# Kernel tuning notes

Hardware: AMD Instinct MI355X
Metric: run time of the kernel (lower is better)

Reference implementation:

```python
import jax, jax.numpy as jnp
from jax import lax
import numpy as np

T, B, DIN, NQ = 256, 2048, 128, 16  # hidden_dim == n_qubits (required by module math)


def setup_inputs() -> dict:
    key = jax.random.key(0)
    k1, k2, k3 = jax.random.split(key, 3)
    inputs = jax.random.normal(k1, (T, B, DIN), dtype=jnp.float32)
    # stacked params for the 4 gates: forget, input, update, output
    W = jax.random.normal(k2, (4, NQ, DIN + NQ), dtype=jnp.float32) * 0.1
    b = jnp.zeros((4, NQ), dtype=jnp.float32)
    theta = jax.random.normal(k3, (4, NQ), dtype=jnp.float32)
    return {"inputs": inputs, "W": W, "b": b, "theta": theta}


def reference(inputs, W, b, theta):
    # Analytic simulation of each QGate circuit:
    #   RX(x_i) then RX(theta_i) on wire i  ->  product state, <Z_i> = cos(x_i + theta_i)
    #   CNOT chain (0->1, 1->2, ...): Heisenberg picture maps Z_k -> Z_0 Z_1 ... Z_k,
    Tn, Bn, _ = inputs.shape
    nq = theta.shape[-1]
    h0 = jnp.zeros((Bn, nq), dtype=inputs.dtype)
    c0 = jnp.zeros((Bn, nq), dtype=inputs.dtype)

    def step(carry, x):
        hx, cx = carry
        combined = jnp.concatenate([x, hx], axis=1)              # [B, Din+H]
        z = jnp.einsum('bd,gnd->bgn', combined, W) + b           # [B, 4, nq]
        q = jnp.cumprod(jnp.cos(z + theta), axis=-1)             # quantum gate expectations
        f = jax.nn.sigmoid(q[:, 0])
        i = jax.nn.sigmoid(q[:, 1])
        g = jnp.tanh(q[:, 2])
        o = jax.nn.sigmoid(q[:, 3])
        cx = f * cx + i * g
        hx = o * jnp.tanh(cx)
        return (hx, cx), hx

    (hx, cx), outputs = lax.scan(step, (h0, c0), inputs)
    return outputs, hx, cx
```

## Files before the change

kernel.cpp:

```cpp
#include <hip/hip_runtime.h>
#include <hip/hip_bf16.h>
#include <stdint.h>


#define T_STEPS 256
#define BATCH   2048
#define DIN     128
#define NQ      16
#define DTOT    144
#define NTILE   32
#define ZROW    66

typedef __attribute__((ext_vector_type(8))) short bf16x8;
typedef __attribute__((ext_vector_type(4))) float f32x4;

__device__ __forceinline__ float bf2f(unsigned short u) {
    union { unsigned int i; float f; } v; v.i = ((unsigned int)u) << 16; return v.f;
}
__device__ __forceinline__ unsigned short f2bf(float f) {
    union { float f; unsigned int i; } v; v.f = f;
    unsigned int i = v.i;
    unsigned int r = i + 0x7fffu + ((i >> 16) & 1u);
    return (unsigned short)(r >> 16);
}
__device__ __forceinline__ float ldval(const float* p) { return *p; }
__device__ __forceinline__ float ldval(const unsigned short* p) { return bf2f(*p); }

__device__ __forceinline__ int detect_bf16(const unsigned int* __restrict__ xw, int lane) {
    int cnt = 0;
#pragma unroll
    for (int i = 0; i < 4; ++i) {
        unsigned int w = xw[lane + i * 64];
        unsigned int e = (w >> 7) & 0xFFu;
        cnt += (e >= 100u && e <= 140u) ? 1 : 0;
    }
#pragma unroll
    for (int d = 32; d > 0; d >>= 1) cnt += __shfl_down(cnt, d, 64);
    int tot = __shfl(cnt, 0, 64);
    return (tot >= 140) ? 1 : 0;
}

template <int CTRL>
__device__ __forceinline__ float dpp_sh(float v) {
    int r = __builtin_amdgcn_update_dpp(__builtin_bit_cast(int, 1.0f),
                                        __builtin_bit_cast(int, v),
                                        CTRL, 0xF, 0xF, false);
    return __builtin_bit_cast(float, r);
}
template <int CTRL>
__device__ __forceinline__ float rot16(float v) {
    int r = __builtin_amdgcn_update_dpp(0, __builtin_bit_cast(int, v),
                                        CTRL, 0xF, 0xF, false);
    return __builtin_bit_cast(float, r);
}

__device__ __forceinline__ float dot1(float h, float cur, const float (&Wp)[16]) {
    float h1  = rot16<0x121>(h), h2  = rot16<0x122>(h), h3  = rot16<0x123>(h);
    float h4  = rot16<0x124>(h), h5  = rot16<0x125>(h), h6  = rot16<0x126>(h), h7  = rot16<0x127>(h);
    float h8  = rot16<0x128>(h), h9  = rot16<0x129>(h), h10 = rot16<0x12A>(h), h11 = rot16<0x12B>(h);
    float h12 = rot16<0x12C>(h), h13 = rot16<0x12D>(h), h14 = rot16<0x12E>(h), h15 = rot16<0x12F>(h);
    float a0 = fmaf(Wp[3], h3, fmaf(Wp[2], h2, fmaf(Wp[1], h1, fmaf(Wp[0], h, cur))));
    float a1 = fmaf(Wp[7], h7, fmaf(Wp[6], h6, fmaf(Wp[5], h5, Wp[4] * h4)));
    float a2 = fmaf(Wp[11], h11, fmaf(Wp[10], h10, fmaf(Wp[9], h9, Wp[8] * h8)));
    float a3 = fmaf(Wp[15], h15, fmaf(Wp[14], h14, fmaf(Wp[13], h13, Wp[12] * h12)));
    return (a0 + a1) + (a2 + a3);
}

template <int BASE>
__device__ __forceinline__ float cosprefix(float z) {
    float cz = __cosf(z);
    cz *= dpp_sh<BASE + 1>(cz);
    cz *= dpp_sh<BASE + 2>(cz);
    cz *= dpp_sh<BASE + 4>(cz);
    cz *= dpp_sh<BASE + 8>(cz);
    return cz;
}

__device__ __forceinline__ void tail1(int t, int g, int n, float cz,
                                      float& h, float& c, float& hs, int b,
                                      float kexp, float ksc, float koff,
                                      int a_f, int a_i, int a_g, int a_o,
                                      float* __restrict__ out)
{
    float e = __builtin_amdgcn_exp2f(cz * kexp);
    float rr = __builtin_amdgcn_rcpf(1.f + e);
    float s = fmaf(ksc, rr, koff);

    int si = __builtin_bit_cast(int, s);
    float fv = __builtin_bit_cast(float, __builtin_amdgcn_ds_bpermute(a_f, si));
    float iv = __builtin_bit_cast(float, __builtin_amdgcn_ds_bpermute(a_i, si));
    float gv = __builtin_bit_cast(float, __builtin_amdgcn_ds_bpermute(a_g, si));
    float ov = __builtin_bit_cast(float, __builtin_amdgcn_ds_bpermute(a_o, si));

    c = fmaf(fv, c, iv * gv);
    float e2 = __builtin_amdgcn_exp2f(c * -2.885390082f);
    float tc = fmaf(2.f, __builtin_amdgcn_rcpf(1.f + e2), -1.f);
    h = ov * tc;

    if ((t & 3) == g) hs = h;
    if ((t & 3) == 3)
        out[(size_t)(t - 3 + g) * (BATCH * NQ) + (size_t)b * NQ + n] = hs;
}

template <int BASE, typename InT>
__device__ __forceinline__ void fused_main(
    const InT* __restrict__ x, const InT* __restrict__ W,
    const InT* __restrict__ bv, const InT* __restrict__ th,
    float* __restrict__ out, int bA, int w, int lane,
    const float (&Wp)[16], float (*zt)[ZROW],
    bf16x8 (*wfh)[64], bf16x8 (*wfl)[64])
{
    const int m = lane & 15, quad = lane >> 4;
    const int g = quad, n = m;
    const int bB = bA + 1;
    const float kexp = (g == 2) ? -2.885390082f : -1.442695041f;
    const float ksc  = (g == 2) ? 2.f : 1.f;
    const float koff = (g == 2) ? -1.f : 0.f;
    const int a_f = n << 2, a_i = (16 + n) << 2, a_g = (32 + n) << 2, a_o = (48 + n) << 2;

    if constexpr (sizeof(InT) == 2) {
#pragma unroll
        for (int nb = 0; nb < 4; ++nb)
            wfh[w * 4 + nb][lane] = *(const bf16x8*)((const unsigned short*)W +
                                    (size_t)(nb * 16 + m) * DTOT + w * 32 + quad * 8);
    } else {
#pragma unroll
        for (int nb = 0; nb < 4; ++nb) {
            const float* p = (const float*)W + (size_t)(nb * 16 + m) * DTOT + w * 32 + quad * 8;
            bf16x8 ah, al;
#pragma unroll
            for (int j = 0; j < 8; ++j) {
                float wv = p[j];
                unsigned short hh = f2bf(wv);
                ah[j] = (short)hh;
                al[j] = (short)f2bf(wv - bf2f(hh));
            }
            wfh[w * 4 + nb][lane] = ah;
            wfl[w * 4 + nb][lane] = al;
        }
    }
    const float bias = ldval(bv + lane) + ldval(th + lane);
    __syncthreads();

    const InT* xbase = x + ((size_t)(m & 7) * BATCH + (size_t)(bA + (m >> 3))) * DIN + quad * 8;

    f32x4 rx[8]; bf16x8 rbx[4];
    auto LOAD = [&](int tl) {
        const InT* p = xbase + (size_t)tl * ((size_t)8 * BATCH * DIN);
#pragma unroll
        for (int kt = 0; kt < 4; ++kt) {
            if constexpr (sizeof(InT) == 2) {
                rbx[kt] = *(const bf16x8*)(p + kt * 32);
            } else {
                rx[2 * kt]     = *(const f32x4*)((const float*)p + kt * 32);
                rx[2 * kt + 1] = *(const f32x4*)((const float*)p + kt * 32 + 4);
            }
        }
    };
    auto PRODUCE = [&]() {
        f32x4 acc[4] = {};
#pragma unroll
        for (int kt = 0; kt < 4; ++kt) {
            if constexpr (sizeof(InT) == 2) {
#pragma unroll
                for (int nb = 0; nb < 4; ++nb)
                    acc[nb] = __builtin_amdgcn_mfma_f32_16x16x32_bf16(rbx[kt], wfh[kt * 4 + nb][lane], acc[nb], 0, 0, 0);
            } else {
                bf16x8 ah, al;
#pragma unroll
                for (int j = 0; j < 8; ++j) {
                    float xv = rx[2 * kt + (j >> 2)][j & 3];
                    unsigned short hh = f2bf(xv);
                    ah[j] = (short)hh;
                    al[j] = (short)f2bf(xv - bf2f(hh));
                }
#pragma unroll
                for (int nb = 0; nb < 4; ++nb)
                    acc[nb] = __builtin_amdgcn_mfma_f32_16x16x32_bf16(ah, wfh[kt * 4 + nb][lane], acc[nb], 0, 0, 0);
#pragma unroll
                for (int nb = 0; nb < 4; ++nb)
                    acc[nb] = __builtin_amdgcn_mfma_f32_16x16x32_bf16(al, wfh[kt * 4 + nb][lane], acc[nb], 0, 0, 0);
#pragma unroll
                for (int nb = 0; nb < 4; ++nb)
                    acc[nb] = __builtin_amdgcn_mfma_f32_16x16x32_bf16(ah, wfl[kt * 4 + nb][lane], acc[nb], 0, 0, 0);
            }
        }
#pragma unroll
        for (int nb = 0; nb < 4; ++nb)
#pragma unroll
            for (int r = 0; r < 4; ++r)
                zt[quad * 4 + r][nb * 16 + m] = acc[nb][r];
    };

    float hA = 0.f, cA = 0.f, hsA = 0.f;
    float hB = 0.f, cB = 0.f, hsB = 0.f;
    float zrA[8], zrB[8];

    LOAD(0);
    PRODUCE();
    LOAD(1);
#pragma unroll
    for (int j = 0; j < 8; ++j) zrA[j] = zt[j][lane] + bias;
#pragma unroll
    for (int j = 0; j < 8; ++j) zrB[j] = zt[8 + j][lane] + bias;

    float zA = dot1(hA, zrA[0], Wp);
    float czB = 0.f;

#pragma unroll 1
    for (int tl = 0; tl < NTILE; ++tl) {
        if (tl < NTILE - 1) PRODUCE();
        if (tl < NTILE - 2) LOAD(tl + 2);
#pragma unroll
        for (int j = 0; j < 8; ++j) {
            const int t = tl * 8 + j;
            float czA = cosprefix<BASE>(zA);
            if (j != 0 || tl != 0)
                tail1(t - 1, g, n, czB, hB, cB, hsB, bB,
                      kexp, ksc, koff, a_f, a_i, a_g, a_o, out);
            float zB = dot1(hB, zrB[j], Wp);
            czB = cosprefix<BASE>(zB);
            tail1(t, g, n, czA, hA, cA, hsA, bA,
                  kexp, ksc, koff, a_f, a_i, a_g, a_o, out);
            if (j < 7) zA = dot1(hA, zrA[j + 1], Wp);
        }
        if (tl < NTILE - 1) {
#pragma unroll
            for (int j = 0; j < 8; ++j) zrA[j] = zt[j][lane] + bias;
#pragma unroll
            for (int j = 0; j < 8; ++j) zrB[j] = zt[8 + j][lane] + bias;
            zA = dot1(hA, zrA[0], Wp);
        }
    }
    tail1(T_STEPS - 1, g, n, czB, hB, cB, hsB, bB,
          kexp, ksc, koff, a_f, a_i, a_g, a_o, out);

    if (g == 0) {
        out[(size_t)T_STEPS * BATCH * NQ + (size_t)bA * NQ + n] = hA;
        out[(size_t)T_STEPS * BATCH * NQ + (size_t)BATCH * NQ + (size_t)bA * NQ + n] = cA;
        out[(size_t)T_STEPS * BATCH * NQ + (size_t)bB * NQ + n] = hB;
        out[(size_t)T_STEPS * BATCH * NQ + (size_t)BATCH * NQ + (size_t)bB * NQ + n] = cB;
    }
}

__global__ __launch_bounds__(256, 1) void qlstm_fused(
    const void* __restrict__ x_, const void* __restrict__ W_,
    const void* __restrict__ b_, const void* __restrict__ th_,
    float* __restrict__ out)
{
    __shared__ float  zw[4][16][ZROW];
    __shared__ bf16x8 wfh[16][64];
    __shared__ bf16x8 wfl[16][64];

    const int lane = threadIdx.x & 63;
    const int w    = threadIdx.x >> 6;
    const int bA   = (blockIdx.x * 4 + w) * 2;
    const int n    = lane & 15;

    const int isbf = __builtin_amdgcn_readfirstlane(detect_bf16((const unsigned int*)x_, lane));

    int pr  = __builtin_amdgcn_update_dpp(0, lane, 0x121, 0xF, 0xF, false);
    int p0r = __shfl(pr, 0, 64);
    const int d = (p0r == 1) ? 1 : 15;

    float Wp[16];
    if (isbf) {
        const unsigned short* W = (const unsigned short*)W_;
#pragma unroll
        for (int k = 0; k < 16; ++k)
            Wp[k] = bf2f(W[(size_t)lane * DTOT + DIN + ((n + k * d) & 15)]);
    } else {
        const float* W = (const float*)W_;
#pragma unroll
        for (int k = 0; k < 16; ++k)
            Wp[k] = W[(size_t)lane * DTOT + DIN + ((n + k * d) & 15)];
    }

    int probe = __builtin_amdgcn_update_dpp(999, lane, 0x111, 0xF, 0xF, false);
    int p2 = __shfl(probe, 2, 64);

    if (isbf) {
        if (p2 == 1) fused_main<0x110, unsigned short>((const unsigned short*)x_, (const unsigned short*)W_,
                                                       (const unsigned short*)b_, (const unsigned short*)th_,
                                                       out, bA, w, lane, Wp, zw[w], wfh, wfl);
        else         fused_main<0x100, unsigned short>((const unsigned short*)x_, (const unsigned short*)W_,
                                                       (const unsigned short*)b_, (const unsigned short*)th_,
                                                       out, bA, w, lane, Wp, zw[w], wfh, wfl);
    } else {
        if (p2 == 1) fused_main<0x110, float>((const float*)x_, (const float*)W_,
                                              (const float*)b_, (const float*)th_,
                                              out, bA, w, lane, Wp, zw[w], wfh, wfl);
        else         fused_main<0x100, float>((const float*)x_, (const float*)W_,
                                              (const float*)b_, (const float*)th_,
                                              out, bA, w, lane, Wp, zw[w], wfh, wfl);
    }
}

extern "C" void kernel_launch(void* const* d_in, const int* in_sizes, int n_in,
                              void* d_out, int out_size, void* d_ws, size_t ws_size,
                              hipStream_t stream) {
    const void* x  = d_in[0];
    const void* W  = d_in[1];
    const void* bv = d_in[2];
    const void* th = d_in[3];
    (void)d_ws; (void)ws_size;
    qlstm_fused<<<BATCH / 8, 256, 0, stream>>>(x, W, bv, th, (float*)d_out);
}
```

Baseline: 397.1 us.

## Remap lanes to four batch rows per wave with all gates per lane

Each wave now handles four batch rows, one per 16-lane quad, and every lane computes all four gates itself. This drops the ds_bpermute gate exchange and the two-row interleaved pipeline in favour of 4x more recurrent FMAs and transcendentals per lane. Blocks shrink to 128 threads, the x tile covers 4 timesteps instead of 8, and outputs are stored every step instead of being batched. The longer per-step serial chain (four cosprefix scans, four sigmoid/tanh calls) and lower occupancy could outweigh the saved cross-lane traffic.

```diff
diff --git a/kernel.cpp b/kernel.cpp
--- a/kernel.cpp
+++ b/kernel.cpp
@@ -8,8 +8,8 @@
 #define DIN     128
 #define NQ      16
 #define DTOT    144
-#define NTILE   32
-#define ZROW    66
+#define NTILE   64
+#define ZROW    70
 
 typedef __attribute__((ext_vector_type(8))) short bf16x8;
 typedef __attribute__((ext_vector_type(4))) float f32x4;
@@ -52,18 +52,6 @@
     int r = __builtin_amdgcn_update_dpp(0, __builtin_bit_cast(int, v),
                                         CTRL, 0xF, 0xF, false);
     return __builtin_bit_cast(float, r);
-}
-
-__device__ __forceinline__ float dot1(float h, float cur, const float (&Wp)[16]) {
-    float h1  = rot16<0x121>(h), h2  = rot16<0x122>(h), h3  = rot16<0x123>(h);
-    float h4  = rot16<0x124>(h), h5  = rot16<0x125>(h), h6  = rot16<0x126>(h), h7  = rot16<0x127>(h);
-    float h8  = rot16<0x128>(h), h9  = rot16<0x129>(h), h10 = rot16<0x12A>(h), h11 = rot16<0x12B>(h);
-    float h12 = rot16<0x12C>(h), h13 = rot16<0x12D>(h), h14 = rot16<0x12E>(h), h15 = rot16<0x12F>(h);
-    float a0 = fmaf(Wp[3], h3, fmaf(Wp[2], h2, fmaf(Wp[1], h1, fmaf(Wp[0], h, cur))));
-    float a1 = fmaf(Wp[7], h7, fmaf(Wp[6], h6, fmaf(Wp[5], h5, Wp[4] * h4)));
-    float a2 = fmaf(Wp[11], h11, fmaf(Wp[10], h10, fmaf(Wp[9], h9, Wp[8] * h8)));
-    float a3 = fmaf(Wp[15], h15, fmaf(Wp[14], h14, fmaf(Wp[13], h13, Wp[12] * h12)));
-    return (a0 + a1) + (a2 + a3);
 }
 
 template <int BASE>
@@ -76,30 +64,47 @@
     return cz;
 }
 
-__device__ __forceinline__ void tail1(int t, int g, int n, float cz,
-                                      float& h, float& c, float& hs, int b,
-                                      float kexp, float ksc, float koff,
-                                      int a_f, int a_i, int a_g, int a_o,
-                                      float* __restrict__ out)
+__device__ __forceinline__ float sigm_(float a) {
+    float e = __builtin_amdgcn_exp2f(a * -1.442695041f);
+    return __builtin_amdgcn_rcpf(1.f + e);
+}
+__device__ __forceinline__ float tanh_(float a) {
+    float e = __builtin_amdgcn_exp2f(a * -2.885390082f);
+    return fmaf(2.f, __builtin_amdgcn_rcpf(1.f + e), -1.f);
+}
+
+template <int BASE>
+__device__ __forceinline__ void qstep4(int t, int b, int n,
+                                       float zb0, float zb1, float zb2, float zb3,
+                                       const float (&Wp)[4][16], float& h, float& c,
+                                       float* __restrict__ out)
 {
-    float e = __builtin_amdgcn_exp2f(cz * kexp);
-    float rr = __builtin_amdgcn_rcpf(1.f + e);
-    float s = fmaf(ksc, rr, koff);
-
-    int si = __builtin_bit_cast(int, s);
-    float fv = __builtin_bit_cast(float, __builtin_amdgcn_ds_bpermute(a_f, si));
-    float iv = __builtin_bit_cast(float, __builtin_amdgcn_ds_bpermute(a_i, si));
-    float gv = __builtin_bit_cast(float, __builtin_amdgcn_ds_bpermute(a_g, si));
-    float ov = __builtin_bit_cast(float, __builtin_amdgcn_ds_bpermute(a_o, si));
+    float h1  = rot16<0x121>(h), h2  = rot16<0x122>(h), h3  = rot16<0x123>(h);
+    float h4  = rot16<0x124>(h), h5  = rot16<0x125>(h), h6  = rot16<0x126>(h), h7  = rot16<0x127>(h);
+    float h8  = rot16<0x128>(h), h9  = rot16<0x129>(h), h10 = rot16<0x12A>(h), h11 = rot16<0x12B>(h);
+    float h12 = rot16<0x12C>(h), h13 = rot16<0x12D>(h), h14 = rot16<0x12E>(h), h15 = rot16<0x12F>(h);
+
+    float zin[4] = {zb0, zb1, zb2, zb3};
+    float cz[4];
+#pragma unroll
+    for (int g = 0; g < 4; ++g) {
+        float a0 = fmaf(Wp[g][3],  h3,  fmaf(Wp[g][2],  h2,  fmaf(Wp[g][1],  h1,  fmaf(Wp[g][0], h, zin[g]))));
+        float a1 = fmaf(Wp[g][7],  h7,  fmaf(Wp[g][6],  h6,  fmaf(Wp[g][5],  h5,  Wp[g][4]  * h4)));
+        float a2 = fmaf(Wp[g][11], h11, fmaf(Wp[g][10], h10, fmaf(Wp[g][9],  h9,  Wp[g][8]  * h8)));
+        float a3 = fmaf(Wp[g][15], h15, fmaf(Wp[g][14], h14, fmaf(Wp[g][13], h13, Wp[g][12] * h12)));
+        cz[g] = cosprefix<BASE>((a0 + a1) + (a2 + a3));
+    }
+
+    float fv = sigm_(cz[0]);
+    float iv = sigm_(cz[1]);
+    float gv = tanh_(cz[2]);
+    float ov = sigm_(cz[3]);
 
     c = fmaf(fv, c, iv * gv);
-    float e2 = __builtin_amdgcn_exp2f(c * -2.885390082f);
-    float tc = fmaf(2.f, __builtin_amdgcn_rcpf(1.f + e2), -1.f);
+    float tc = tanh_(c);
     h = ov * tc;
 
-    if ((t & 3) == g) hs = h;
-    if ((t & 3) == 3)
-        out[(size_t)(t - 3 + g) * (BATCH * NQ) + (size_t)b * NQ + n] = hs;
+    out[(size_t)t * (BATCH * NQ) + (size_t)b * NQ + n] = h;
 }
 
 template <int BASE, typename InT>
@@ -107,46 +112,49 @@
     const InT* __restrict__ x, const InT* __restrict__ W,
     const InT* __restrict__ bv, const InT* __restrict__ th,
     float* __restrict__ out, int bA, int w, int lane,
-    const float (&Wp)[16], float (*zt)[ZROW],
+    const float (&Wp)[4][16], float (*zt)[ZROW],
     bf16x8 (*wfh)[64], bf16x8 (*wfl)[64])
 {
     const int m = lane & 15, quad = lane >> 4;
-    const int g = quad, n = m;
-    const int bB = bA + 1;
-    const float kexp = (g == 2) ? -2.885390082f : -1.442695041f;
-    const float ksc  = (g == 2) ? 2.f : 1.f;
-    const float koff = (g == 2) ? -1.f : 0.f;
-    const int a_f = n << 2, a_i = (16 + n) << 2, a_g = (32 + n) << 2, a_o = (48 + n) << 2;
-
-    if constexpr (sizeof(InT) == 2) {
-#pragma unroll
-        for (int nb = 0; nb < 4; ++nb)
-            wfh[w * 4 + nb][lane] = *(const bf16x8*)((const unsigned short*)W +
-                                    (size_t)(nb * 16 + m) * DTOT + w * 32 + quad * 8);
-    } else {
-#pragma unroll
-        for (int nb = 0; nb < 4; ++nb) {
-            const float* p = (const float*)W + (size_t)(nb * 16 + m) * DTOT + w * 32 + quad * 8;
-            bf16x8 ah, al;
-#pragma unroll
-            for (int j = 0; j < 8; ++j) {
-                float wv = p[j];
-                unsigned short hh = f2bf(wv);
-                ah[j] = (short)hh;
-                al[j] = (short)f2bf(wv - bf2f(hh));
+    const int beta = quad, n = m;
+    const int b = bA + beta;
+
+#pragma unroll
+    for (int kk = 0; kk < 2; ++kk) {
+        const int kt = 2 * w + kk;
+        if constexpr (sizeof(InT) == 2) {
+#pragma unroll
+            for (int nb = 0; nb < 4; ++nb)
+                wfh[kt * 4 + nb][lane] = *(const bf16x8*)((const unsigned short*)W +
+                                         (size_t)(nb * 16 + m) * DTOT + kt * 32 + quad * 8);
+        } else {
+#pragma unroll
+            for (int nb = 0; nb < 4; ++nb) {
+                const float* p = (const float*)W + (size_t)(nb * 16 + m) * DTOT + kt * 32 + quad * 8;
+                bf16x8 ah, al;
+#pragma unroll
+                for (int j = 0; j < 8; ++j) {
+                    float wv = p[j];
+                    unsigned short hh = f2bf(wv);
+                    ah[j] = (short)hh;
+                    al[j] = (short)f2bf(wv - bf2f(hh));
+                }
+                wfh[kt * 4 + nb][lane] = ah;
+                wfl[kt * 4 + nb][lane] = al;
             }
-            wfh[w * 4 + nb][lane] = ah;
-            wfl[w * 4 + nb][lane] = al;
         }
     }
-    const float bias = ldval(bv + lane) + ldval(th + lane);
+    float bias[4];
+#pragma unroll
+    for (int g = 0; g < 4; ++g)
+        bias[g] = ldval(bv + g * 16 + n) + ldval(th + g * 16 + n);
     __syncthreads();
 
-    const InT* xbase = x + ((size_t)(m & 7) * BATCH + (size_t)(bA + (m >> 3))) * DIN + quad * 8;
+    const InT* xbase = x + ((size_t)(m >> 2) * BATCH + (size_t)(bA + (m & 3))) * DIN + quad * 8;
 
     f32x4 rx[8]; bf16x8 rbx[4];
     auto LOAD = [&](int tl) {
-        const InT* p = xbase + (size_t)tl * ((size_t)8 * BATCH * DIN);
+        const InT* p = xbase + (size_t)tl * ((size_t)4 * BATCH * DIN);
 #pragma unroll
         for (int kt = 0; kt < 4; ++kt) {
             if constexpr (sizeof(InT) == 2) {
@@ -192,69 +200,45 @@
                 zt[quad * 4 + r][nb * 16 + m] = acc[nb][r];
     };
 
-    float hA = 0.f, cA = 0.f, hsA = 0.f;
-    float hB = 0.f, cB = 0.f, hsB = 0.f;
-    float zrA[8], zrB[8];
+    float h = 0.f, c = 0.f;
 
     LOAD(0);
     PRODUCE();
     LOAD(1);
-#pragma unroll
-    for (int j = 0; j < 8; ++j) zrA[j] = zt[j][lane] + bias;
-#pragma unroll
-    for (int j = 0; j < 8; ++j) zrB[j] = zt[8 + j][lane] + bias;
-
-    float zA = dot1(hA, zrA[0], Wp);
-    float czB = 0.f;
 
 #pragma unroll 1
     for (int tl = 0; tl < NTILE; ++tl) {
+        float zr[16];
+#pragma unroll
+        for (int tt = 0; tt < 4; ++tt)
+#pragma unroll
+            for (int g = 0; g < 4; ++g)
+                zr[tt * 4 + g] = zt[tt * 4 + beta][g * 16 + n] + bias[g];
         if (tl < NTILE - 1) PRODUCE();
         if (tl < NTILE - 2) LOAD(tl + 2);
 #pragma unroll
-        for (int j = 0; j < 8; ++j) {
-            const int t = tl * 8 + j;
-            float czA = cosprefix<BASE>(zA);
-            if (j != 0 || tl != 0)
-                tail1(t - 1, g, n, czB, hB, cB, hsB, bB,
-                      kexp, ksc, koff, a_f, a_i, a_g, a_o, out);
-            float zB = dot1(hB, zrB[j], Wp);
-            czB = cosprefix<BASE>(zB);
-            tail1(t, g, n, czA, hA, cA, hsA, bA,
-                  kexp, ksc, koff, a_f, a_i, a_g, a_o, out);
-            if (j < 7) zA = dot1(hA, zrA[j + 1], Wp);
-        }
-        if (tl < NTILE - 1) {
-#pragma unroll
-            for (int j = 0; j < 8; ++j) zrA[j] = zt[j][lane] + bias;
-#pragma unroll
-            for (int j = 0; j < 8; ++j) zrB[j] = zt[8 + j][lane] + bias;
-            zA = dot1(hA, zrA[0], Wp);
-        }
-    }
-    tail1(T_STEPS - 1, g, n, czB, hB, cB, hsB, bB,
-          kexp, ksc, koff, a_f, a_i, a_g, a_o, out);
-
-    if (g == 0) {
-        out[(size_t)T_STEPS * BATCH * NQ + (size_t)bA * NQ + n] = hA;
-        out[(size_t)T_STEPS * BATCH * NQ + (size_t)BATCH * NQ + (size_t)bA * NQ + n] = cA;
-        out[(size_t)T_STEPS * BATCH * NQ + (size_t)bB * NQ + n] = hB;
-        out[(size_t)T_STEPS * BATCH * NQ + (size_t)BATCH * NQ + (size_t)bB * NQ + n] = cB;
-    }
-}
-
-__global__ __launch_bounds__(256, 1) void qlstm_fused(
+        for (int tt = 0; tt < 4; ++tt)
+            qstep4<BASE>(tl * 4 + tt, b, n,
+                         zr[tt * 4 + 0], zr[tt * 4 + 1], zr[tt * 4 + 2], zr[tt * 4 + 3],
+                         Wp, h, c, out);
+    }
+
+    out[(size_t)T_STEPS * BATCH * NQ + (size_t)b * NQ + n] = h;
+    out[(size_t)T_STEPS * BATCH * NQ + (size_t)BATCH * NQ + (size_t)b * NQ + n] = c;
+}
+
+__global__ __launch_bounds__(128, 1) void qlstm_fused(
     const void* __restrict__ x_, const void* __restrict__ W_,
     const void* __restrict__ b_, const void* __restrict__ th_,
     float* __restrict__ out)
 {
-    __shared__ float  zw[4][16][ZROW];
+    __shared__ float  zw[2][16][ZROW];
     __shared__ bf16x8 wfh[16][64];
     __shared__ bf16x8 wfl[16][64];
 
     const int lane = threadIdx.x & 63;
     const int w    = threadIdx.x >> 6;
-    const int bA   = (blockIdx.x * 4 + w) * 2;
+    const int bA   = (blockIdx.x * 2 + w) * 4;
     const int n    = lane & 15;
 
     const int isbf = __builtin_amdgcn_readfirstlane(detect_bf16((const unsigned int*)x_, lane));
@@ -263,17 +247,21 @@
     int p0r = __shfl(pr, 0, 64);
     const int d = (p0r == 1) ? 1 : 15;
 
-    float Wp[16];
+    float Wp[4][16];
     if (isbf) {
         const unsigned short* W = (const unsigned short*)W_;
 #pragma unroll
-        for (int k = 0; k < 16; ++k)
-            Wp[k] = bf2f(W[(size_t)lane * DTOT + DIN + ((n + k * d) & 15)]);
+        for (int g = 0; g < 4; ++g)
+#pragma unroll
+            for (int k = 0; k < 16; ++k)
+                Wp[g][k] = bf2f(W[(size_t)(g * 16 + n) * DTOT + DIN + ((n + k * d) & 15)]);
     } else {
         const float* W = (const float*)W_;
 #pragma unroll
-        for (int k = 0; k < 16; ++k)
-            Wp[k] = W[(size_t)lane * DTOT + DIN + ((n + k * d) & 15)];
+        for (int g = 0; g < 4; ++g)
+#pragma unroll
+            for (int k = 0; k < 16; ++k)
+                Wp[g][k] = W[(size_t)(g * 16 + n) * DTOT + DIN + ((n + k * d) & 15)];
     }
 
     int probe = __builtin_amdgcn_update_dpp(999, lane, 0x111, 0xF, 0xF, false);
@@ -304,5 +292,5 @@
     const void* bv = d_in[2];
     const void* th = d_in[3];
     (void)d_ws; (void)ws_size;
-    qlstm_fused<<<BATCH / 8, 256, 0, stream>>>(x, W, bv, th, (float*)d_out);
-}
+    qlstm_fused<<<BATCH / 8, 128, 0, stream>>>(x, W, bv, th, (float*)d_out);
+}
```

After: 429.3 us. +8.1%, slower.
